# Kernel tuning notes

Hardware: AMD Instinct MI355X
Metric: run time of the kernel (lower is better)

## Reference

```python
import jax, jax.numpy as jnp
from jax import lax
import numpy as np

N_TOOLS = 50
DIM = 512
N_TOKENS = 8192
PARAM_DIM = 256


def setup_inputs() -> dict:
    key = jax.random.key(0)
    ks = jax.random.split(key, 8)
    s = 1.0 / np.sqrt(DIM)
    x = jax.random.normal(ks[0], (N_TOKENS, DIM), dtype=jnp.float32)
    router_w = jax.random.uniform(ks[1], (N_TOOLS, DIM), jnp.float32, -s, s)
    router_b = jax.random.uniform(ks[2], (N_TOOLS,), jnp.float32, -s, s)
    expert_w = jax.random.uniform(ks[3], (N_TOOLS, DIM, DIM), jnp.float32, -s, s)
    expert_b = jax.random.uniform(ks[4], (N_TOOLS, DIM), jnp.float32, -s, s)
    param_w = jax.random.uniform(ks[5], (PARAM_DIM, DIM), jnp.float32, -s, s)
    param_b = jax.random.uniform(ks[6], (PARAM_DIM,), jnp.float32, -s, s)
    return {"x": x, "router_w": router_w, "router_b": router_b,
            "expert_w": expert_w, "expert_b": expert_b,
            "param_w": param_w, "param_b": param_b}


def _moe_adapt(x, tool_idx, expert_w, expert_b):
    # Top-1 dispatch: for each expert i, y_i = x @ W_i.T + b_i, written only
    # where tool_idx == i. Scan over the fixed 50 experts (mirrors the torch
    # masked per-expert Linear loop) with masked select instead of scatter.
    def step(acc, wb):
        i, W, b = wb
        y = x @ W.T + b  # [N, dim]
        mask = (tool_idx == i)[:, None]
        return jnp.where(mask, y, acc), None

    init = jnp.zeros_like(x)
    acc, _ = lax.scan(step, init, (jnp.arange(N_TOOLS), expert_w, expert_b))
    return acc


def reference(x, router_w, router_b, expert_w, expert_b, param_w, param_b):
    tool_logits = x @ router_w.T + router_b            # [N, 50]
    tool_probs = jax.nn.softmax(tool_logits, axis=-1)   # [N, 50]
    tool_idx = jnp.argmax(tool_probs, axis=-1)          # [N] int
    adapted = _moe_adapt(x, tool_idx, expert_w, expert_b)  # [N, dim]
    params = x @ param_w.T + param_b                    # [N, 256]
    return (tool_idx, tool_probs, adapted, params)
```

## Files before the change

### kernel.cpp

```cpp
#include <hip/hip_runtime.h>
#include <hip/hip_bf16.h>
#include <math.h>

#define N_TOKENS 8192
#define DIM      512
#define N_TOOLS  50
#define PARAM_DIM 256
#define N_ROWBLK (N_TOKENS / 64)
#define MAX_BATCHES 128
#define LDSS 72

typedef float  f32x4 __attribute__((ext_vector_type(4)));
typedef short  s16x8 __attribute__((ext_vector_type(8)));
typedef short  s16x4 __attribute__((ext_vector_type(4)));

#define WS_IDX     0
#define WS_HIST    8192
#define WS_PHIST   14592
#define WS_OFFSETS 20992
#define WS_COUNTS  21056
#define WS_ORDER   21120
#define WS_BE      29312
#define WS_BM0     29504
#define WS_NB      29696
#define WS_XH      32768
#define WS_XL      2130944

__device__ inline float bf2f(short s) {
    return __uint_as_float(((unsigned)(unsigned short)s) << 16);
}

__device__ inline s16x4 pk4(float a, float b, float c, float d) {
    __hip_bfloat162 p0 = __float22bfloat162_rn(make_float2(a, b));
    __hip_bfloat162 p1 = __float22bfloat162_rn(make_float2(c, d));
    union { __hip_bfloat162 h; short2 s; } u0, u1;
    u0.h = p0; u1.h = p1;
    s16x4 r; r[0] = u0.s.x; r[1] = u0.s.y; r[2] = u1.s.x; r[3] = u1.s.y;
    return r;
}

__global__ __launch_bounds__(256) void cvt_x_kernel(const float* __restrict__ x,
                                                    short* __restrict__ xh,
                                                    short* __restrict__ xl) {
    size_t i = (size_t)(blockIdx.x * 256 + threadIdx.x) * 4;
    float4 v = *(const float4*)&x[i];
    s16x4 h = pk4(v.x, v.y, v.z, v.w);
    s16x4 l = pk4(v.x - bf2f(h[0]), v.y - bf2f(h[1]),
                  v.z - bf2f(h[2]), v.w - bf2f(h[3]));
    *(s16x4*)&xh[i] = h;
    *(s16x4*)&xl[i] = l;
}

__global__ __launch_bounds__(256) void head_mfma(const short* __restrict__ xh,
                                                 const short* __restrict__ xl,
                                                 const float* __restrict__ pw,
                                                 const float* __restrict__ pb,
                                                 const float* __restrict__ rw,
                                                 const float* __restrict__ rb,
                                                 float* __restrict__ out_params,
                                                 float* __restrict__ probs,
                                                 float* __restrict__ out_idx,
                                                 int* __restrict__ idx_i,
                                                 int* __restrict__ hist) {
    int r0 = blockIdx.y * 64;
    bool isl = (blockIdx.x == 4);
    int c0 = isl ? 0 : blockIdx.x * 64;

    __shared__ short As[64 * LDSS];
    __shared__ short Bs[64 * LDSS];
    __shared__ short Al[64 * LDSS];
    __shared__ short Bl[64 * LDSS];
    __shared__ int rowcol[64];

    int tid = threadIdx.x;
    int wv = tid >> 6;
    int lane = tid & 63;
    int fm = lane & 15;
    int q = lane >> 4;

    const float* Bsrc = isl ? rw : pw;

    int ar0 = tid >> 3, ag = tid & 7;
    int ar1 = ar0 + 32;
    const short* aptr0  = xh + (size_t)(r0 + ar0) * DIM + ag * 8;
    const short* aptr1  = xh + (size_t)(r0 + ar1) * DIM + ag * 8;
    const short* alptr0 = xl + (size_t)(r0 + ar0) * DIM + ag * 8;
    const short* alptr1 = xl + (size_t)(r0 + ar1) * DIM + ag * 8;
    int bc[4], bg[4];
    const float* bptr[4];
#pragma unroll
    for (int i = 0; i < 4; ++i) {
        int u = i * 256 + tid;
        bc[i] = u >> 4; bg[i] = u & 15;
        bptr[i] = Bsrc + (size_t)bc[i] * DIM + c0 * (isl ? 0 : 1) * 0 + (size_t)0;
        bptr[i] = Bsrc + (size_t)(c0 + bc[i]) * DIM + bg[i] * 4;
    }

    f32x4 acc[4] = {{0.f, 0.f, 0.f, 0.f}, {0.f, 0.f, 0.f, 0.f},
                    {0.f, 0.f, 0.f, 0.f}, {0.f, 0.f, 0.f, 0.f}};

    s16x8 apre0, apre1, alpre0, alpre1;
    float4 bpre[4];
    apre0 = *(const s16x8*)aptr0;
    apre1 = *(const s16x8*)aptr1;
    if (isl) { alpre0 = *(const s16x8*)alptr0; alpre1 = *(const s16x8*)alptr1; }
#pragma unroll
    for (int i = 0; i < 4; ++i) {
        float4 v = {0.f, 0.f, 0.f, 0.f};
        if (!isl || bc[i] < N_TOOLS) v = *(const float4*)bptr[i];
        bpre[i] = v;
    }

    for (int k0 = 0; k0 < DIM; k0 += 64) {
        *(s16x8*)&As[ar0 * LDSS + ag * 8] = apre0;
        *(s16x8*)&As[ar1 * LDSS + ag * 8] = apre1;
        if (isl) {
            *(s16x8*)&Al[ar0 * LDSS + ag * 8] = alpre0;
            *(s16x8*)&Al[ar1 * LDSS + ag * 8] = alpre1;
        }
#pragma unroll
        for (int i = 0; i < 4; ++i) {
            float4 v = bpre[i];
            s16x4 h = pk4(v.x, v.y, v.z, v.w);
            *(s16x4*)&Bs[bc[i] * LDSS + bg[i] * 4] = h;
            if (isl) {
                s16x4 l = pk4(v.x - bf2f(h[0]), v.y - bf2f(h[1]),
                              v.z - bf2f(h[2]), v.w - bf2f(h[3]));
                *(s16x4*)&Bl[bc[i] * LDSS + bg[i] * 4] = l;
            }
        }
        __syncthreads();

        int kn = k0 + 64;
        if (kn < DIM) {
            apre0 = *(const s16x8*)(aptr0 + kn);
            apre1 = *(const s16x8*)(aptr1 + kn);
            if (isl) {
                alpre0 = *(const s16x8*)(alptr0 + kn);
                alpre1 = *(const s16x8*)(alptr1 + kn);
            }
#pragma unroll
            for (int i = 0; i < 4; ++i) {
                float4 v = {0.f, 0.f, 0.f, 0.f};
                if (!isl || bc[i] < N_TOOLS) v = *(const float4*)(bptr[i] + kn);
                bpre[i] = v;
            }
        }

#pragma unroll
        for (int kk = 0; kk < 64; kk += 32) {
            int ao = (wv * 16 + fm) * LDSS + kk + q * 8;
            s16x8 a = *(const s16x8*)&As[ao];
            if (!isl) {
#pragma unroll
                for (int n = 0; n < 4; ++n) {
                    s16x8 b = *(const s16x8*)&Bs[(n * 16 + fm) * LDSS + kk + q * 8];
                    acc[n] = __builtin_amdgcn_mfma_f32_16x16x32_bf16(a, b, acc[n], 0, 0, 0);
                }
            } else {
                s16x8 al = *(const s16x8*)&Al[ao];
#pragma unroll
                for (int n = 0; n < 4; ++n) {
                    int bo = (n * 16 + fm) * LDSS + kk + q * 8;
                    s16x8 b  = *(const s16x8*)&Bs[bo];
                    s16x8 bl = *(const s16x8*)&Bl[bo];
                    acc[n] = __builtin_amdgcn_mfma_f32_16x16x32_bf16(a,  b,  acc[n], 0, 0, 0);
                    acc[n] = __builtin_amdgcn_mfma_f32_16x16x32_bf16(a,  bl, acc[n], 0, 0, 0);
                    acc[n] = __builtin_amdgcn_mfma_f32_16x16x32_bf16(al, b,  acc[n], 0, 0, 0);
                }
            }
        }
        __syncthreads();
    }

    if (!isl) {
        float bias[4];
#pragma unroll
        for (int n = 0; n < 4; ++n) bias[n] = pb[c0 + n * 16 + fm];
#pragma unroll
        for (int r = 0; r < 4; ++r) {
            int row = r0 + wv * 16 + q * 4 + r;
            float* op = out_params + (size_t)row * PARAM_DIM + c0;
#pragma unroll
            for (int n = 0; n < 4; ++n) op[n * 16 + fm] = acc[n][r] + bias[n];
        }
    } else {
        float rbv[4];
#pragma unroll
        for (int n = 0; n < 4; ++n) {
            int c = n * 16 + fm;
            rbv[n] = (c < N_TOOLS) ? rb[c] : 0.f;
        }
#pragma unroll
        for (int rr = 0; rr < 4; ++rr) {
            int row_l = wv * 16 + q * 4 + rr;
            int row = r0 + row_l;
            float v[4];
            float vmax = -INFINITY; int vcol = N_TOOLS;
#pragma unroll
            for (int n = 0; n < 4; ++n) {
                int c = n * 16 + fm;
                v[n] = acc[n][rr] + rbv[n];
                if (c < N_TOOLS && v[n] > vmax) { vmax = v[n]; vcol = c; }
            }
#pragma unroll
            for (int s = 1; s < 16; s <<= 1) {
                float om = __shfl_xor(vmax, s, 64);
                int   oc = __shfl_xor(vcol, s, 64);
                if (om > vmax || (om == vmax && oc < vcol)) { vmax = om; vcol = oc; }
            }
            float e[4]; float esum = 0.f;
#pragma unroll
            for (int n = 0; n < 4; ++n) {
                int c = n * 16 + fm;
                e[n] = (c < N_TOOLS) ? expf(v[n] - vmax) : 0.f;
                esum += e[n];
            }
#pragma unroll
            for (int s = 1; s < 16; s <<= 1) esum += __shfl_xor(esum, s, 64);
            float inv = 1.f / esum;
#pragma unroll
            for (int n = 0; n < 4; ++n) {
                int c = n * 16 + fm;
                if (c < N_TOOLS) probs[(size_t)row * N_TOOLS + c] = e[n] * inv;
            }
            if (fm == 0) {
                out_idx[row] = (float)vcol;
                idx_i[row] = vcol;
                rowcol[row_l] = vcol;
            }
        }
        __syncthreads();
        if (wv == 0) {
            int myc = rowcol[lane];
            int cnt = 0;
            for (int e2 = 0; e2 < N_TOOLS; ++e2) {
                unsigned long long m = __ballot(myc == e2);
                if (lane == e2) cnt = __popcll(m);
            }
            if (lane < N_TOOLS) hist[blockIdx.y * N_TOOLS + lane] = cnt;
        }
    }
}

__global__ __launch_bounds__(1024) void scan_all(const int* __restrict__ hist,
                                                 int* __restrict__ phist,
                                                 int* __restrict__ counts,
                                                 int* __restrict__ offsets,
                                                 int* __restrict__ batch_e,
                                                 int* __restrict__ batch_m0,
                                                 int* __restrict__ nb_out) {
    __shared__ int cnt_s[64];
    int l = threadIdx.x & 63;
    int w = threadIdx.x >> 6;

    for (int e = w; e < N_TOOLS; e += 16) {
        int v0 = hist[l * N_TOOLS + e];
        int v1 = hist[(64 + l) * N_TOOLS + e];
        int s0 = v0;
#pragma unroll
        for (int s = 1; s < 64; s <<= 1) {
            int t = __shfl_up(s0, s, 64);
            if (l >= s) s0 += t;
        }
        int tot0 = __shfl(s0, 63, 64);
        int s1 = v1;
#pragma unroll
        for (int s = 1; s < 64; s <<= 1) {
            int t = __shfl_up(s1, s, 64);
            if (l >= s) s1 += t;
        }
        s1 += tot0;
        phist[l * N_TOOLS + e] = s0 - v0;
        phist[(64 + l) * N_TOOLS + e] = s1 - v1;
        if (l == 63) cnt_s[e] = s1;
    }
    __syncthreads();

    if (w == 0) {
        int c = (l < N_TOOLS) ? cnt_s[l] : 0;
        int pre = c;
#pragma unroll
        for (int s = 1; s < 64; s <<= 1) {
            int v = __shfl_up(pre, s, 64);
            if (l >= s) pre += v;
        }
        if (l < N_TOOLS) { offsets[l] = pre - c; counts[l] = c; }

        int nb_i = (l < N_TOOLS) ? (c + 127) >> 7 : 0;
        int pre2 = nb_i;
#pragma unroll
        for (int s = 1; s < 64; s <<= 1) {
            int v = __shfl_up(pre2, s, 64);
            if (l >= s) pre2 += v;
        }
        int bstart = pre2 - nb_i;
        for (int b = 0; b < nb_i; ++b) {
            batch_e[bstart + b] = l;
            batch_m0[bstart + b] = b * 128;
        }
        if (l == 63) nb_out[0] = pre2;
    }
}

__global__ void reorder_kernel(const int* __restrict__ idx_i,
                               const int* __restrict__ offsets,
                               const int* __restrict__ phist,
                               int* __restrict__ order) {
    int b = blockIdx.x;
    int lane = threadIdx.x;
    int t = b * 64 + lane;
    int e = idx_i[t];
    unsigned long long lt = (1ull << lane) - 1ull;
    int rank = 0;
    for (int ex = 0; ex < N_TOOLS; ++ex) {
        unsigned long long m = __ballot(e == ex);
        if (e == ex) rank = __popcll(m & lt);
    }
    order[offsets[e] + phist[b * N_TOOLS + e] + rank] = t;
}

__global__ __launch_bounds__(256) void adapted_mfma(const short* __restrict__ xh,
                                                    const float* __restrict__ ew,
                                                    const float* __restrict__ eb,
                                                    const int* __restrict__ order,
                                                    const int* __restrict__ batch_e,
                                                    const int* __restrict__ batch_m0,
                                                    const int* __restrict__ nb_ptr,
                                                    const int* __restrict__ offsets,
                                                    const int* __restrict__ counts,
                                                    float* __restrict__ out) {
    int b = blockIdx.y;
    if (b >= nb_ptr[0]) return;
    int e = batch_e[b];
    int m0 = batch_m0[b];
    int c0 = blockIdx.x * 128;
    int start = offsets[e] + m0;
    int len = counts[e] - m0;
    if (len > 128) len = 128;

    __shared__ short As[128 * LDSS];
    __shared__ short Bs[128 * LDSS];
    __shared__ int toks[128];

    int tid = threadIdx.x;
    if (tid < 128) toks[tid] = (tid < len) ? order[start + tid] : -1;
    __syncthreads();

    int wv = tid >> 6;
    int lane = tid & 63;
    int fm = lane & 15;
    int q = lane >> 4;

    const float* We = ew + (size_t)e * DIM * DIM;

    int arb = tid >> 3, ag = tid & 7;
    const short* aptr[4];
#pragma unroll
    for (int i = 0; i < 4; ++i) {
        int tok = toks[arb + 32 * i];
        aptr[i] = (tok >= 0) ? xh + (size_t)tok * DIM + ag * 8 : nullptr;
    }
    int bcb = tid >> 4, bg = tid & 15;
    const float* bptr[8];
#pragma unroll
    for (int i = 0; i < 8; ++i)
        bptr[i] = We + (size_t)(c0 + bcb + 16 * i) * DIM + bg * 4;

    f32x4 acc[2][8];
#pragma unroll
    for (int m = 0; m < 2; ++m)
#pragma unroll
        for (int n = 0; n < 8; ++n) acc[m][n] = {0.f, 0.f, 0.f, 0.f};

    const s16x8 z8 = {0, 0, 0, 0, 0, 0, 0, 0};
    s16x8 apre[4];
    float4 bpre[8];
#pragma unroll
    for (int i = 0; i < 4; ++i) apre[i] = aptr[i] ? *(const s16x8*)aptr[i] : z8;
#pragma unroll
    for (int i = 0; i < 8; ++i) bpre[i] = *(const float4*)bptr[i];

    for (int k0 = 0; k0 < DIM; k0 += 64) {
#pragma unroll
        for (int i = 0; i < 4; ++i)
            *(s16x8*)&As[(arb + 32 * i) * LDSS + ag * 8] = apre[i];
#pragma unroll
        for (int i = 0; i < 8; ++i) {
            float4 v = bpre[i];
            *(s16x4*)&Bs[(bcb + 16 * i) * LDSS + bg * 4] = pk4(v.x, v.y, v.z, v.w);
        }
        __syncthreads();

        int kn = k0 + 64;
        if (kn < DIM) {
#pragma unroll
            for (int i = 0; i < 4; ++i)
                apre[i] = aptr[i] ? *(const s16x8*)(aptr[i] + kn) : z8;
#pragma unroll
            for (int i = 0; i < 8; ++i) bpre[i] = *(const float4*)(bptr[i] + kn);
        }

#pragma unroll
        for (int kk = 0; kk < 64; kk += 32) {
            s16x8 a[2];
#pragma unroll
            for (int m = 0; m < 2; ++m)
                a[m] = *(const s16x8*)&As[(wv * 32 + m * 16 + fm) * LDSS + kk + q * 8];
#pragma unroll
            for (int n = 0; n < 8; ++n) {
                s16x8 bf = *(const s16x8*)&Bs[(n * 16 + fm) * LDSS + kk + q * 8];
#pragma unroll
                for (int m = 0; m < 2; ++m)
                    acc[m][n] = __builtin_amdgcn_mfma_f32_16x16x32_bf16(a[m], bf, acc[m][n], 0, 0, 0);
            }
        }
        __syncthreads();
    }

    float bias[8];
#pragma unroll
    for (int n = 0; n < 8; ++n) bias[n] = eb[(size_t)e * DIM + c0 + n * 16 + fm];

#pragma unroll
    for (int m = 0; m < 2; ++m)
#pragma unroll
        for (int r = 0; r < 4; ++r) {
            int row = wv * 32 + m * 16 + q * 4 + r;
            int tok = toks[row];
            if (tok < 0) continue;
            float* op = out + (size_t)tok * DIM + c0;
#pragma unroll
            for (int n = 0; n < 8; ++n) op[n * 16 + fm] = acc[m][n][r] + bias[n];
        }
}

extern "C" void kernel_launch(void* const* d_in, const int* in_sizes, int n_in,
                              void* d_out, int out_size, void* d_ws, size_t ws_size,
                              hipStream_t stream) {
    const float* x        = (const float*)d_in[0];
    const float* router_w = (const float*)d_in[1];
    const float* router_b = (const float*)d_in[2];
    const float* expert_w = (const float*)d_in[3];
    const float* expert_b = (const float*)d_in[4];
    const float* param_w  = (const float*)d_in[5];
    const float* param_b  = (const float*)d_in[6];

    float* out = (float*)d_out;
    float* out_idx     = out;
    float* out_probs   = out + N_TOKENS;
    float* out_adapted = out + N_TOKENS + N_TOKENS * N_TOOLS;
    float* out_params  = out_adapted + (size_t)N_TOKENS * DIM;

    int* ws = (int*)d_ws;
    int* ws_idx     = ws + WS_IDX;
    int* ws_hist    = ws + WS_HIST;
    int* ws_phist   = ws + WS_PHIST;
    int* ws_offsets = ws + WS_OFFSETS;
    int* ws_counts  = ws + WS_COUNTS;
    int* ws_order   = ws + WS_ORDER;
    int* ws_be      = ws + WS_BE;
    int* ws_bm0     = ws + WS_BM0;
    int* ws_nb      = ws + WS_NB;
    short* ws_xh    = (short*)(ws + WS_XH);
    short* ws_xl    = (short*)(ws + WS_XL);

    cvt_x_kernel<<<N_TOKENS * DIM / 4 / 256, 256, 0, stream>>>(x, ws_xh, ws_xl);

    head_mfma<<<dim3(5, N_ROWBLK), 256, 0, stream>>>(ws_xh, ws_xl, param_w, param_b,
                                                     router_w, router_b,
                                                     out_params, out_probs,
                                                     out_idx, ws_idx, ws_hist);

    scan_all<<<1, 1024, 0, stream>>>(ws_hist, ws_phist, ws_counts, ws_offsets,
                                     ws_be, ws_bm0, ws_nb);

    reorder_kernel<<<N_ROWBLK, 64, 0, stream>>>(ws_idx, ws_offsets, ws_phist, ws_order);

    adapted_mfma<<<dim3(4, MAX_BATCHES), 256, 0, stream>>>(ws_xh, expert_w, expert_b,
                                                           ws_order, ws_be, ws_bm0, ws_nb,
                                                           ws_offsets, ws_counts, out_adapted);
}
```

Before: 159.4 us.

## Pre-convert expert and param weights to bf16, load A fragments directly from global

Result: slower. 164.5 us (+3.2%).

```diff
diff --git a/kernel.cpp b/kernel.cpp
--- a/kernel.cpp
+++ b/kernel.cpp
@@ -7,7 +7,7 @@
 #define N_TOOLS  50
 #define PARAM_DIM 256
 #define N_ROWBLK (N_TOKENS / 64)
-#define MAX_BATCHES 128
+#define MAX_BATCHES 192
 #define LDSS 72
 
 typedef float  f32x4 __attribute__((ext_vector_type(4)));
@@ -24,7 +24,14 @@
 #define WS_BM0     29504
 #define WS_NB      29696
 #define WS_XH      32768
-#define WS_XL      2130944
+#define WS_XL      (WS_XH + 2097152)
+#define WS_EWH     (WS_XL + 2097152)
+#define WS_PWH     (WS_EWH + 6553600)
+
+#define X4   1048576
+#define EW4  3276800
+#define PW4  32768
+#define TOT4 (X4 + EW4 + PW4)
 
 __device__ inline float bf2f(short s) {
     return __uint_as_float(((unsigned)(unsigned short)s) << 16);
@@ -39,21 +46,36 @@
     return r;
 }
 
-__global__ __launch_bounds__(256) void cvt_x_kernel(const float* __restrict__ x,
-                                                    short* __restrict__ xh,
-                                                    short* __restrict__ xl) {
-    size_t i = (size_t)(blockIdx.x * 256 + threadIdx.x) * 4;
-    float4 v = *(const float4*)&x[i];
-    s16x4 h = pk4(v.x, v.y, v.z, v.w);
-    s16x4 l = pk4(v.x - bf2f(h[0]), v.y - bf2f(h[1]),
-                  v.z - bf2f(h[2]), v.w - bf2f(h[3]));
-    *(s16x4*)&xh[i] = h;
-    *(s16x4*)&xl[i] = l;
+__global__ __launch_bounds__(256) void cvt_all(const float* __restrict__ x,
+                                               const float* __restrict__ ew,
+                                               const float* __restrict__ pw,
+                                               short* __restrict__ xh,
+                                               short* __restrict__ xl,
+                                               short* __restrict__ ewh,
+                                               short* __restrict__ pwh) {
+    size_t u = (size_t)blockIdx.x * 256 + threadIdx.x;
+    if (u < X4) {
+        size_t i = u * 4;
+        float4 v = *(const float4*)&x[i];
+        s16x4 h = pk4(v.x, v.y, v.z, v.w);
+        s16x4 l = pk4(v.x - bf2f(h[0]), v.y - bf2f(h[1]),
+                      v.z - bf2f(h[2]), v.w - bf2f(h[3]));
+        *(s16x4*)&xh[i] = h;
+        *(s16x4*)&xl[i] = l;
+    } else if (u < X4 + EW4) {
+        size_t i = (u - X4) * 4;
+        float4 v = *(const float4*)&ew[i];
+        *(s16x4*)&ewh[i] = pk4(v.x, v.y, v.z, v.w);
+    } else {
+        size_t i = (u - X4 - EW4) * 4;
+        float4 v = *(const float4*)&pw[i];
+        *(s16x4*)&pwh[i] = pk4(v.x, v.y, v.z, v.w);
+    }
 }
 
 __global__ __launch_bounds__(256) void head_mfma(const short* __restrict__ xh,
                                                  const short* __restrict__ xl,
-                                                 const float* __restrict__ pw,
+                                                 const short* __restrict__ pwh,
                                                  const float* __restrict__ pb,
                                                  const float* __restrict__ rw,
                                                  const float* __restrict__ rb,
@@ -66,9 +88,7 @@
     bool isl = (blockIdx.x == 4);
     int c0 = isl ? 0 : blockIdx.x * 64;
 
-    __shared__ short As[64 * LDSS];
     __shared__ short Bs[64 * LDSS];
-    __shared__ short Al[64 * LDSS];
     __shared__ short Bl[64 * LDSS];
     __shared__ int rowcol[64];
 
@@ -78,113 +98,132 @@
     int fm = lane & 15;
     int q = lane >> 4;
 
-    const float* Bsrc = isl ? rw : pw;
-
-    int ar0 = tid >> 3, ag = tid & 7;
-    int ar1 = ar0 + 32;
-    const short* aptr0  = xh + (size_t)(r0 + ar0) * DIM + ag * 8;
-    const short* aptr1  = xh + (size_t)(r0 + ar1) * DIM + ag * 8;
-    const short* alptr0 = xl + (size_t)(r0 + ar0) * DIM + ag * 8;
-    const short* alptr1 = xl + (size_t)(r0 + ar1) * DIM + ag * 8;
-    int bc[4], bg[4];
-    const float* bptr[4];
-#pragma unroll
-    for (int i = 0; i < 4; ++i) {
-        int u = i * 256 + tid;
-        bc[i] = u >> 4; bg[i] = u & 15;
-        bptr[i] = Bsrc + (size_t)bc[i] * DIM + c0 * (isl ? 0 : 1) * 0 + (size_t)0;
-        bptr[i] = Bsrc + (size_t)(c0 + bc[i]) * DIM + bg[i] * 4;
-    }
+    const short* aph = xh + (size_t)(r0 + wv * 16 + fm) * DIM + q * 8;
+    const short* apl = xl + (size_t)(r0 + wv * 16 + fm) * DIM + q * 8;
 
     f32x4 acc[4] = {{0.f, 0.f, 0.f, 0.f}, {0.f, 0.f, 0.f, 0.f},
                     {0.f, 0.f, 0.f, 0.f}, {0.f, 0.f, 0.f, 0.f}};
-
-    s16x8 apre0, apre1, alpre0, alpre1;
-    float4 bpre[4];
-    apre0 = *(const s16x8*)aptr0;
-    apre1 = *(const s16x8*)aptr1;
-    if (isl) { alpre0 = *(const s16x8*)alptr0; alpre1 = *(const s16x8*)alptr1; }
-#pragma unroll
-    for (int i = 0; i < 4; ++i) {
-        float4 v = {0.f, 0.f, 0.f, 0.f};
-        if (!isl || bc[i] < N_TOOLS) v = *(const float4*)bptr[i];
-        bpre[i] = v;
-    }
-
-    for (int k0 = 0; k0 < DIM; k0 += 64) {
-        *(s16x8*)&As[ar0 * LDSS + ag * 8] = apre0;
-        *(s16x8*)&As[ar1 * LDSS + ag * 8] = apre1;
-        if (isl) {
-            *(s16x8*)&Al[ar0 * LDSS + ag * 8] = alpre0;
-            *(s16x8*)&Al[ar1 * LDSS + ag * 8] = alpre1;
-        }
-#pragma unroll
-        for (int i = 0; i < 4; ++i) {
-            float4 v = bpre[i];
-            s16x4 h = pk4(v.x, v.y, v.z, v.w);
-            *(s16x4*)&Bs[bc[i] * LDSS + bg[i] * 4] = h;
-            if (isl) {
-                s16x4 l = pk4(v.x - bf2f(h[0]), v.y - bf2f(h[1]),
-                              v.z - bf2f(h[2]), v.w - bf2f(h[3]));
-                *(s16x4*)&Bl[bc[i] * LDSS + bg[i] * 4] = l;
-            }
-        }
-        __syncthreads();
-
-        int kn = k0 + 64;
-        if (kn < DIM) {
-            apre0 = *(const s16x8*)(aptr0 + kn);
-            apre1 = *(const s16x8*)(aptr1 + kn);
-            if (isl) {
-                alpre0 = *(const s16x8*)(alptr0 + kn);
-                alpre1 = *(const s16x8*)(alptr1 + kn);
-            }
-#pragma unroll
-            for (int i = 0; i < 4; ++i) {
-                float4 v = {0.f, 0.f, 0.f, 0.f};
-                if (!isl || bc[i] < N_TOOLS) v = *(const float4*)(bptr[i] + kn);
-                bpre[i] = v;
-            }
-        }
-
-#pragma unroll
-        for (int kk = 0; kk < 64; kk += 32) {
-            int ao = (wv * 16 + fm) * LDSS + kk + q * 8;
-            s16x8 a = *(const s16x8*)&As[ao];
-            if (!isl) {
+    const s16x8 z8 = {0, 0, 0, 0, 0, 0, 0, 0};
+
+    if (!isl) {
+        int col[2], g[2];
+        const short* bptr[2];
+#pragma unroll
+        for (int i = 0; i < 2; ++i) {
+            int u = i * 256 + tid;
+            col[i] = u >> 3; g[i] = u & 7;
+            bptr[i] = pwh + (size_t)(c0 + col[i]) * DIM + g[i] * 8;
+        }
+        s16x8 bpre[2];
+#pragma unroll
+        for (int i = 0; i < 2; ++i) bpre[i] = *(const s16x8*)bptr[i];
+        s16x8 a0 = *(const s16x8*)aph;
+        s16x8 a1 = *(const s16x8*)(aph + 32);
+
+        for (int k0 = 0; k0 < DIM; k0 += 64) {
+#pragma unroll
+            for (int i = 0; i < 2; ++i)
+                *(s16x8*)&Bs[col[i] * LDSS + g[i] * 8] = bpre[i];
+            __syncthreads();
+
+            int kn = k0 + 64;
+            s16x8 a0n = z8, a1n = z8;
+            if (kn < DIM) {
+#pragma unroll
+                for (int i = 0; i < 2; ++i) bpre[i] = *(const s16x8*)(bptr[i] + kn);
+                a0n = *(const s16x8*)(aph + kn);
+                a1n = *(const s16x8*)(aph + kn + 32);
+            }
+
+#pragma unroll
+            for (int kk = 0; kk < 64; kk += 32) {
+                s16x8 a = kk ? a1 : a0;
 #pragma unroll
                 for (int n = 0; n < 4; ++n) {
                     s16x8 b = *(const s16x8*)&Bs[(n * 16 + fm) * LDSS + kk + q * 8];
                     acc[n] = __builtin_amdgcn_mfma_f32_16x16x32_bf16(a, b, acc[n], 0, 0, 0);
                 }
-            } else {
-                s16x8 al = *(const s16x8*)&Al[ao];
+            }
+            __syncthreads();
+            a0 = a0n; a1 = a1n;
+        }
+
+        float bias[4];
+#pragma unroll
+        for (int n = 0; n < 4; ++n) bias[n] = pb[c0 + n * 16 + fm];
+#pragma unroll
+        for (int r = 0; r < 4; ++r) {
+            int row = r0 + wv * 16 + q * 4 + r;
+            float* op = out_params + (size_t)row * PARAM_DIM + c0;
+#pragma unroll
+            for (int n = 0; n < 4; ++n) op[n * 16 + fm] = acc[n][r] + bias[n];
+        }
+    } else {
+        int col[4], g[4];
+        const float* bptr[4];
+#pragma unroll
+        for (int i = 0; i < 4; ++i) {
+            int u = i * 256 + tid;
+            col[i] = u >> 4; g[i] = u & 15;
+            bptr[i] = rw + (size_t)col[i] * DIM + g[i] * 4;
+        }
+        float4 bpre[4];
+#pragma unroll
+        for (int i = 0; i < 4; ++i) {
+            float4 v = {0.f, 0.f, 0.f, 0.f};
+            if (col[i] < N_TOOLS) v = *(const float4*)bptr[i];
+            bpre[i] = v;
+        }
+        s16x8 a0h = *(const s16x8*)aph;
+        s16x8 a1h = *(const s16x8*)(aph + 32);
+        s16x8 a0l = *(const s16x8*)apl;
+        s16x8 a1l = *(const s16x8*)(apl + 32);
+
+        for (int k0 = 0; k0 < DIM; k0 += 64) {
+#pragma unroll
+            for (int i = 0; i < 4; ++i) {
+                float4 v = bpre[i];
+                s16x4 h = pk4(v.x, v.y, v.z, v.w);
+                *(s16x4*)&Bs[col[i] * LDSS + g[i] * 4] = h;
+                s16x4 l = pk4(v.x - bf2f(h[0]), v.y - bf2f(h[1]),
+                              v.z - bf2f(h[2]), v.w - bf2f(h[3]));
+                *(s16x4*)&Bl[col[i] * LDSS + g[i] * 4] = l;
+            }
+            __syncthreads();
+
+            int kn = k0 + 64;
+            s16x8 a0hn = z8, a1hn = z8, a0ln = z8, a1ln = z8;
+            if (kn < DIM) {
+#pragma unroll
+                for (int i = 0; i < 4; ++i) {
+                    float4 v = {0.f, 0.f, 0.f, 0.f};
+                    if (col[i] < N_TOOLS) v = *(const float4*)(bptr[i] + kn);
+                    bpre[i] = v;
+                }
+                a0hn = *(const s16x8*)(aph + kn);
+                a1hn = *(const s16x8*)(aph + kn + 32);
+                a0ln = *(const s16x8*)(apl + kn);
+                a1ln = *(const s16x8*)(apl + kn + 32);
+            }
+
+#pragma unroll
+            for (int kk = 0; kk < 64; kk += 32) {
+                s16x8 ah = kk ? a1h : a0h;
+                s16x8 al = kk ? a1l : a0l;
 #pragma unroll
                 for (int n = 0; n < 4; ++n) {
                     int bo = (n * 16 + fm) * LDSS + kk + q * 8;
                     s16x8 b  = *(const s16x8*)&Bs[bo];
                     s16x8 bl = *(const s16x8*)&Bl[bo];
-                    acc[n] = __builtin_amdgcn_mfma_f32_16x16x32_bf16(a,  b,  acc[n], 0, 0, 0);
-                    acc[n] = __builtin_amdgcn_mfma_f32_16x16x32_bf16(a,  bl, acc[n], 0, 0, 0);
+                    acc[n] = __builtin_amdgcn_mfma_f32_16x16x32_bf16(ah, b,  acc[n], 0, 0, 0);
+                    acc[n] = __builtin_amdgcn_mfma_f32_16x16x32_bf16(ah, bl, acc[n], 0, 0, 0);
                     acc[n] = __builtin_amdgcn_mfma_f32_16x16x32_bf16(al, b,  acc[n], 0, 0, 0);
                 }
             }
-        }
-        __syncthreads();
-    }
-
-    if (!isl) {
-        float bias[4];
-#pragma unroll
-        for (int n = 0; n < 4; ++n) bias[n] = pb[c0 + n * 16 + fm];
-#pragma unroll
-        for (int r = 0; r < 4; ++r) {
-            int row = r0 + wv * 16 + q * 4 + r;
-            float* op = out_params + (size_t)row * PARAM_DIM + c0;
-#pragma unroll
-            for (int n = 0; n < 4; ++n) op[n * 16 + fm] = acc[n][r] + bias[n];
-        }
-    } else {
+            __syncthreads();
+            a0h = a0hn; a1h = a1hn; a0l = a0ln; a1l = a1ln;
+        }
+
         float rbv[4];
 #pragma unroll
         for (int n = 0; n < 4; ++n) {
@@ -287,7 +326,7 @@
         }
         if (l < N_TOOLS) { offsets[l] = pre - c; counts[l] = c; }
 
-        int nb_i = (l < N_TOOLS) ? (c + 127) >> 7 : 0;
+        int nb_i = (l < N_TOOLS) ? (c + 63) >> 6 : 0;
         int pre2 = nb_i;
 #pragma unroll
         for (int s = 1; s < 64; s <<= 1) {
@@ -297,7 +336,7 @@
         int bstart = pre2 - nb_i;
         for (int b = 0; b < nb_i; ++b) {
             batch_e[bstart + b] = l;
-            batch_m0[bstart + b] = b * 128;
+            batch_m0[bstart + b] = b * 64;
         }
         if (l == 63) nb_out[0] = pre2;
     }
@@ -321,7 +360,7 @@
 }
 
 __global__ __launch_bounds__(256) void adapted_mfma(const short* __restrict__ xh,
-                                                    const float* __restrict__ ew,
+                                                    const short* __restrict__ ewh,
                                                     const float* __restrict__ eb,
                                                     const int* __restrict__ order,
                                                     const int* __restrict__ batch_e,
@@ -337,14 +376,13 @@
     int c0 = blockIdx.x * 128;
     int start = offsets[e] + m0;
     int len = counts[e] - m0;
-    if (len > 128) len = 128;
-
-    __shared__ short As[128 * LDSS];
+    if (len > 64) len = 64;
+
     __shared__ short Bs[128 * LDSS];
-    __shared__ int toks[128];
+    __shared__ int toks[64];
 
     int tid = threadIdx.x;
-    if (tid < 128) toks[tid] = (tid < len) ? order[start + tid] : -1;
+    if (tid < 64) toks[tid] = (tid < len) ? order[start + tid] : -1;
     __syncthreads();
 
     int wv = tid >> 6;
@@ -352,70 +390,57 @@
     int fm = lane & 15;
     int q = lane >> 4;
 
-    const float* We = ew + (size_t)e * DIM * DIM;
-
-    int arb = tid >> 3, ag = tid & 7;
-    const short* aptr[4];
+    const short* Wb = ewh + (size_t)e * DIM * DIM;
+
+    int col[4], g[4];
+    const short* bptr[4];
 #pragma unroll
     for (int i = 0; i < 4; ++i) {
-        int tok = toks[arb + 32 * i];
-        aptr[i] = (tok >= 0) ? xh + (size_t)tok * DIM + ag * 8 : nullptr;
-    }
-    int bcb = tid >> 4, bg = tid & 15;
-    const float* bptr[8];
-#pragma unroll
-    for (int i = 0; i < 8; ++i)
-        bptr[i] = We + (size_t)(c0 + bcb + 16 * i) * DIM + bg * 4;
-
-    f32x4 acc[2][8];
-#pragma unroll
-    for (int m = 0; m < 2; ++m)
-#pragma unroll
-        for (int n = 0; n < 8; ++n) acc[m][n] = {0.f, 0.f, 0.f, 0.f};
-
+        int u = i * 256 + tid;
+        col[i] = u >> 3; g[i] = u & 7;
+        bptr[i] = Wb + (size_t)(c0 + col[i]) * DIM + g[i] * 8;
+    }
+
+    int tok = toks[wv * 16 + fm];
+    const short* aph = xh + (size_t)(tok >= 0 ? tok : 0) * DIM + q * 8;
+
+    f32x4 acc[8];
+#pragma unroll
+    for (int n = 0; n < 8; ++n) acc[n] = {0.f, 0.f, 0.f, 0.f};
     const s16x8 z8 = {0, 0, 0, 0, 0, 0, 0, 0};
-    s16x8 apre[4];
-    float4 bpre[8];
-#pragma unroll
-    for (int i = 0; i < 4; ++i) apre[i] = aptr[i] ? *(const s16x8*)aptr[i] : z8;
-#pragma unroll
-    for (int i = 0; i < 8; ++i) bpre[i] = *(const float4*)bptr[i];
+
+    s16x8 bpre[4];
+#pragma unroll
+    for (int i = 0; i < 4; ++i) bpre[i] = *(const s16x8*)bptr[i];
+    s16x8 a0 = *(const s16x8*)aph;
+    s16x8 a1 = *(const s16x8*)(aph + 32);
 
     for (int k0 = 0; k0 < DIM; k0 += 64) {
 #pragma unroll
         for (int i = 0; i < 4; ++i)
-            *(s16x8*)&As[(arb + 32 * i) * LDSS + ag * 8] = apre[i];
-#pragma unroll
-        for (int i = 0; i < 8; ++i) {
-            float4 v = bpre[i];
-            *(s16x4*)&Bs[(bcb + 16 * i) * LDSS + bg * 4] = pk4(v.x, v.y, v.z, v.w);
-        }
+            *(s16x8*)&Bs[col[i] * LDSS + g[i] * 8] = bpre[i];
         __syncthreads();
 
         int kn = k0 + 64;
+        s16x8 a0n = z8, a1n = z8;
         if (kn < DIM) {
 #pragma unroll
-            for (int i = 0; i < 4; ++i)
-                apre[i] = aptr[i] ? *(const s16x8*)(aptr[i] + kn) : z8;
-#pragma unroll
-            for (int i = 0; i < 8; ++i) bpre[i] = *(const float4*)(bptr[i] + kn);
+            for (int i = 0; i < 4; ++i) bpre[i] = *(const s16x8*)(bptr[i] + kn);
+            a0n = *(const s16x8*)(aph + kn);
+            a1n = *(const s16x8*)(aph + kn + 32);
         }
 
 #pragma unroll
         for (int kk = 0; kk < 64; kk += 32) {
-            s16x8 a[2];
-#pragma unroll
-            for (int m = 0; m < 2; ++m)
-                a[m] = *(const s16x8*)&As[(wv * 32 + m * 16 + fm) * LDSS + kk + q * 8];
+            s16x8 a = kk ? a1 : a0;
 #pragma unroll
             for (int n = 0; n < 8; ++n) {
                 s16x8 bf = *(const s16x8*)&Bs[(n * 16 + fm) * LDSS + kk + q * 8];
-#pragma unroll
-                for (int m = 0; m < 2; ++m)
-                    acc[m][n] = __builtin_amdgcn_mfma_f32_16x16x32_bf16(a[m], bf, acc[m][n], 0, 0, 0);
+                acc[n] = __builtin_amdgcn_mfma_f32_16x16x32_bf16(a, bf, acc[n], 0, 0, 0);
             }
         }
         __syncthreads();
+        a0 = a0n; a1 = a1n;
     }
 
     float bias[8];
@@ -423,16 +448,14 @@
     for (int n = 0; n < 8; ++n) bias[n] = eb[(size_t)e * DIM + c0 + n * 16 + fm];
 
 #pragma unroll
-    for (int m = 0; m < 2; ++m)
-#pragma unroll
-        for (int r = 0; r < 4; ++r) {
-            int row = wv * 32 + m * 16 + q * 4 + r;
-            int tok = toks[row];
-            if (tok < 0) continue;
-            float* op = out + (size_t)tok * DIM + c0;
-#pragma unroll
-            for (int n = 0; n < 8; ++n) op[n * 16 + fm] = acc[m][n][r] + bias[n];
-        }
+    for (int r = 0; r < 4; ++r) {
+        int row_l = wv * 16 + q * 4 + r;
+        int tk = toks[row_l];
+        if (tk < 0) continue;
+        float* op = out + (size_t)tk * DIM + c0;
+#pragma unroll
+        for (int n = 0; n < 8; ++n) op[n * 16 + fm] = acc[n][r] + bias[n];
+    }
 }
 
 extern "C" void kernel_launch(void* const* d_in, const int* in_sizes, int n_in,
@@ -464,10 +487,13 @@
     int* ws_nb      = ws + WS_NB;
     short* ws_xh    = (short*)(ws + WS_XH);
     short* ws_xl    = (short*)(ws + WS_XL);
-
-    cvt_x_kernel<<<N_TOKENS * DIM / 4 / 256, 256, 0, stream>>>(x, ws_xh, ws_xl);
-
-    head_mfma<<<dim3(5, N_ROWBLK), 256, 0, stream>>>(ws_xh, ws_xl, param_w, param_b,
+    short* ws_ewh   = (short*)(ws + WS_EWH);
+    short* ws_pwh   = (short*)(ws + WS_PWH);
+
+    cvt_all<<<TOT4 / 256, 256, 0, stream>>>(x, expert_w, param_w,
+                                            ws_xh, ws_xl, ws_ewh, ws_pwh);
+
+    head_mfma<<<dim3(5, N_ROWBLK), 256, 0, stream>>>(ws_xh, ws_xl, ws_pwh, param_b,
                                                      router_w, router_b,
                                                      out_params, out_probs,
                                                      out_idx, ws_idx, ws_hist);
@@ -477,7 +503,7 @@
 
     reorder_kernel<<<N_ROWBLK, 64, 0, stream>>>(ws_idx, ws_offsets, ws_phist, ws_order);
 
-    adapted_mfma<<<dim3(4, MAX_BATCHES), 256, 0, stream>>>(ws_xh, expert_w, expert_b,
+    adapted_mfma<<<dim3(4, MAX_BATCHES), 256, 0, stream>>>(ws_xh, ws_ewh, expert_b,
                                                            ws_order, ws_be, ws_bm0, ws_nb,
                                                            ws_offsets, ws_counts, out_adapted);
 }
```
